# Kernel tuning notes

Hardware: AMD Instinct MI355X
Metric: run time of the kernel (lower is better)

The kernel has to match this reference:

```python
import jax, jax.numpy as jnp
import numpy as np

B, S, IN, OUT, SPLIT = 4, 2048, 4096, 4096, 1024


def setup_inputs() -> dict:
    key = jax.random.key(0)
    ks = jax.random.split(key, 14)
    def n(k, shape, scale=1.0):
        return jax.random.normal(k, shape, dtype=jnp.float32) * scale
    return {
        "x": n(ks[0], (B, S, IN)),
        "V": n(ks[1], (SPLIT, IN)),
        "U": n(ks[2], (OUT, SPLIT)),
        "v2": n(ks[3], (1, IN), 0.05),
        "v1": n(ks[4], (1, SPLIT), 0.05),
        "u2": n(ks[5], (1, SPLIT), 0.05),
        "u1": n(ks[6], (1, OUT), 0.05),
        "V_R": n(ks[7], (SPLIT, IN)),
        "U_R": n(ks[8], (OUT, SPLIT)),
        "v2_R": n(ks[9], (1, IN), 0.05),
        "v1_R": n(ks[10], (1, SPLIT), 0.05),
        "u2_R": n(ks[11], (1, SPLIT), 0.05),
        "u1_R": n(ks[12], (1, OUT), 0.05),
        "bias": n(ks[13], (OUT,), 0.02),
    }


def _quantize(w):
    # ITQ binarization: sign(w) with straight-through estimator semantics
    return w + jax.lax.stop_gradient(jnp.sign(w) - w)


def _compute_forward(x2d, V, U, v2, v1, u2, u1):
    # x2d: [T, in]; V: [split, in]; U: [out, split]
    Vq = _quantize(V)
    Uq = _quantize(U)
    v1u2 = v1 * u2  # [1, split]
    h = (x2d * v2) @ Vq.T          # [T, split]
    return (h * v1u2) @ Uq.T * u1  # [T, out]


def reference(x, V, U, v2, v1, u2, u1, V_R, U_R, v2_R, v1_R, u2_R, u1_R, bias):
    lead = x.shape[:-1]
    x2d = x.reshape(-1, x.shape[-1])
    y = _compute_forward(x2d, V, U, v2, v1, u2, u1)
    y = y + _compute_forward(x2d, V_R, U_R, v2_R, v1_R, u2_R, u1_R)
    y = y + bias
    return y.reshape(lead + (U.shape[0],))
```

## Files before the change

kernel.cpp:

```cpp
#include <hip/hip_runtime.h>


typedef __bf16 bf16x8 __attribute__((ext_vector_type(8)));
typedef float floatx4 __attribute__((ext_vector_type(4)));

__device__ __forceinline__ unsigned short f2bf_rne(float f) {
    union { float f; unsigned u; } v; v.f = f;
    unsigned r = v.u + 0x7FFFu + ((v.u >> 16) & 1u);
    return (unsigned short)(r >> 16);
}

__device__ __forceinline__ float sgnf(float w) {
    return (float)((w > 0.f) - (w < 0.f));
}

__device__ __forceinline__ void async_copy16(const void* g, void* l) {
    __builtin_amdgcn_global_load_lds(
        (const __attribute__((address_space(1))) void*)g,
        (__attribute__((address_space(3))) void*)l, 16, 0, 0);
}

#define FENCE() asm volatile("" ::: "memory")
#define BAR() do { FENCE(); __builtin_amdgcn_s_barrier(); FENCE(); } while (0)
#define VMW(N) asm volatile("s_waitcnt vmcnt(" #N ")" ::: "memory")
#define LGKM(N) asm volatile("s_waitcnt lgkmcnt(" #N ")" ::: "memory")


__global__ void prep_all_kernel(const float* __restrict__ x,
                                unsigned short* __restrict__ xb,
                                const float* __restrict__ V, const float* __restrict__ V_R,
                                const float* __restrict__ v2, const float* __restrict__ v2_R,
                                const float* __restrict__ U, const float* __restrict__ U_R,
                                const float* __restrict__ v1, const float* __restrict__ v1_R,
                                const float* __restrict__ u2, const float* __restrict__ u2_R,
                                const float* __restrict__ u1, const float* __restrict__ u1_R,
                                unsigned short* __restrict__ W1,
                                unsigned short* __restrict__ W2) {
    int bid = blockIdx.x;
    if (bid < 32768) {
        int i = bid * blockDim.x + threadIdx.x;
        float4 v = ((const float4*)x)[i];
        ushort4 o;
        o.x = f2bf_rne(v.x); o.y = f2bf_rne(v.y);
        o.z = f2bf_rne(v.z); o.w = f2bf_rne(v.w);
        ((ushort4*)xb)[i] = o;
    } else if (bid < 40960) {
        int i = (bid - 32768) * blockDim.x + threadIdx.x;
        int idx = i << 2;
        int scat = idx >> 12;
        int k = idx & 4095;
        const float* Vp; const float* sp;
        if (scat < 1024) { Vp = V + ((size_t)scat << 12); sp = v2; }
        else             { Vp = V_R + ((size_t)(scat - 1024) << 12); sp = v2_R; }
        float4 w = *(const float4*)(Vp + k);
        float4 s = *(const float4*)(sp + k);
        ushort4 o;
        o.x = f2bf_rne(sgnf(w.x) * s.x);
        o.y = f2bf_rne(sgnf(w.y) * s.y);
        o.z = f2bf_rne(sgnf(w.z) * s.z);
        o.w = f2bf_rne(sgnf(w.w) * s.w);
        ((ushort4*)W1)[i] = o;
    } else {
        int i = (bid - 40960) * blockDim.x + threadIdx.x;
        int idx = i << 2;
        int o = idx >> 11;
        int scat = idx & 2047;
        int branch = scat >> 10;
        int s = scat & 1023;
        const float* Up  = branch ? U_R  : U;
        const float* v1p = branch ? v1_R : v1;
        const float* u2p = branch ? u2_R : u2;
        float u1v = (branch ? u1_R : u1)[o];
        float4 w = *(const float4*)(Up + ((size_t)o << 10) + s);
        float4 a = *(const float4*)(v1p + s);
        float4 b = *(const float4*)(u2p + s);
        ushort4 out;
        out.x = f2bf_rne(sgnf(w.x) * a.x * b.x * u1v);
        out.y = f2bf_rne(sgnf(w.y) * a.y * b.y * u1v);
        out.z = f2bf_rne(sgnf(w.z) * a.z * b.z * u1v);
        out.w = f2bf_rne(sgnf(w.w) * a.w * b.w * u1v);
        ((ushort4*)W2)[i] = out;
    }
}


template <bool OUT_BF16, bool ADD_BIAS>
__global__ __launch_bounds__(512, 2)
void gemm256(const unsigned short* __restrict__ A,
             const unsigned short* __restrict__ B,
             void* __restrict__ Cv,
             const float* __restrict__ bias,
             int M, int N, int K, int ntn) {
    (void)M;
    __shared__ __align__(16) unsigned short As[2][2][128 * 64];
    __shared__ __align__(16) unsigned short Bs[2][2][128 * 64];

    const int tid = threadIdx.x;
    const int lane = tid & 63;
    const int wave = tid >> 6;
    const int warp_m = wave >> 2;
    const int warp_n = wave & 3;

    const int nwg = gridDim.x;
    const int hw = blockIdx.x;
    const int swz = (hw & 7) * (nwg >> 3) + (hw >> 3);
    const int tm = swz / ntn;
    const int tn = swz - tm * ntn;
    const int m0 = tm << 8;
    const int n0 = tn << 8;

    const int srow = tid >> 3;
    const int scg8 = (((tid & 7) ^ (srow & 7)) << 3);
    const int ldst = tid << 3;
    const size_t Ks = (size_t)K;

    auto stA = [&](int buf, int h, int kt) {
        const unsigned short* g = A + (size_t)(m0 + (h << 7) + srow) * Ks + (kt << 6) + scg8;
        async_copy16(g,             &As[buf][h][ldst]);
        async_copy16(g + (Ks << 6), &As[buf][h][4096 + ldst]);
    };
    auto stB = [&](int buf, int h, int kt) {
        const unsigned short* g = B + (size_t)(n0 + (h << 7) + srow) * Ks + (kt << 6) + scg8;
        async_copy16(g,             &Bs[buf][h][ldst]);
        async_copy16(g + (Ks << 6), &Bs[buf][h][4096 + ldst]);
    };

    const int fm = lane & 15;
    const int cgl = lane >> 4;
    const int key = fm & 7;
    const int ok0 = ((cgl ^ key) << 3);
    const int ok1 = (((4 | cgl) ^ key) << 3);

    auto lda = [&](bf16x8 (&dst)[4][2], int buf, int mh) {
        const unsigned short* base = &As[buf][warp_m][0];
#pragma unroll
        for (int mi = 0; mi < 4; ++mi) {
            const unsigned short* p = base + (((mh << 6) + (mi << 4) + fm) << 6);
            dst[mi][0] = *(const bf16x8*)(p + ok0);
            dst[mi][1] = *(const bf16x8*)(p + ok1);
        }
    };
    auto ldb = [&](bf16x8 (&dst)[2][2], int buf, int nh) {
        const unsigned short* base = &Bs[buf][warp_n >> 1][0];
#pragma unroll
        for (int ni = 0; ni < 2; ++ni) {
            const unsigned short* p = base + ((((warp_n & 1) << 6) + (nh << 5) + (ni << 4) + fm) << 6);
            dst[ni][0] = *(const bf16x8*)(p + ok0);
            dst[ni][1] = *(const bf16x8*)(p + ok1);
        }
    };

    floatx4 acc[8][4];
#pragma unroll
    for (int i = 0; i < 8; ++i)
#pragma unroll
        for (int j = 0; j < 4; ++j)
#pragma unroll
            for (int r = 0; r < 4; ++r) acc[i][j][r] = 0.f;

    bf16x8 a0[4][2], a1[4][2], b0[2][2], b1[2][2];

#define MMAQ(aS, bS, MH, NH) do { \
    __builtin_amdgcn_s_setprio(1); \
    _Pragma("unroll") \
    for (int mi_ = 0; mi_ < 4; ++mi_) { \
      _Pragma("unroll") \
      for (int ni_ = 0; ni_ < 2; ++ni_) { \
        acc[(MH)*4 + mi_][(NH)*2 + ni_] = __builtin_amdgcn_mfma_f32_16x16x32_bf16( \
            aS[mi_][0], bS[ni_][0], acc[(MH)*4 + mi_][(NH)*2 + ni_], 0, 0, 0); \
        acc[(MH)*4 + mi_][(NH)*2 + ni_] = __builtin_amdgcn_mfma_f32_16x16x32_bf16( \
            aS[mi_][1], bS[ni_][1], acc[(MH)*4 + mi_][(NH)*2 + ni_], 0, 0, 0); \
      } } \
    __builtin_amdgcn_s_setprio(0); \
  } while (0)

    stB(0, 0, 0); stB(0, 1, 0); stA(0, 0, 0); stA(0, 1, 0);
    stB(1, 0, 1); stB(1, 1, 1);
    VMW(4);
    BAR();

    const int NT = K >> 6;
    for (int i = 0; i < (NT >> 1) - 1; ++i) {
        const int t1k = 2 * i + 1, t2k = 2 * i + 2, t3k = 2 * i + 3;
        lda(a0, 0, 0); ldb(b0, 0, 0);
        stA(1, 0, t1k);
        LGKM(8);
        BAR(); LGKM(0);
        MMAQ(a0, b0, 0, 0);
        BAR();
        ldb(b1, 0, 1);
        stA(1, 1, t1k);
        BAR(); LGKM(0);
        MMAQ(a0, b1, 0, 1);
        BAR();
        lda(a1, 0, 1);
        stB(0, 0, t2k);
        BAR(); LGKM(0);
        MMAQ(a1, b1, 1, 1);
        BAR();
        stB(0, 1, t2k);
        VMW(4);
        BAR();
        MMAQ(a1, b0, 1, 0);
        BAR();
        lda(a0, 1, 0); ldb(b0, 1, 0);
        stA(0, 0, t2k);
        LGKM(8);
        BAR(); LGKM(0);
        MMAQ(a0, b0, 0, 0);
        BAR();
        ldb(b1, 1, 1);
        stA(0, 1, t2k);
        BAR(); LGKM(0);
        MMAQ(a0, b1, 0, 1);
        BAR();
        lda(a1, 1, 1);
        stB(1, 0, t3k);
        BAR(); LGKM(0);
        MMAQ(a1, b1, 1, 1);
        BAR();
        stB(1, 1, t3k);
        VMW(4);
        BAR();
        MMAQ(a1, b0, 1, 0);
        BAR();
    }
    {
        const int tLk = NT - 1;
        lda(a0, 0, 0); ldb(b0, 0, 0);
        stA(1, 0, tLk);
        LGKM(8);
        BAR(); LGKM(0);
        MMAQ(a0, b0, 0, 0);
        BAR();
        ldb(b1, 0, 1);
        stA(1, 1, tLk);
        BAR(); LGKM(0);
        MMAQ(a0, b1, 0, 1);
        BAR();
        lda(a1, 0, 1);
        BAR(); LGKM(0);
        MMAQ(a1, b1, 1, 1);
        BAR();
        VMW(0);
        BAR();
        MMAQ(a1, b0, 1, 0);
        BAR();
        lda(a0, 1, 0); ldb(b0, 1, 0);
        ldb(b1, 1, 1); lda(a1, 1, 1);
        MMAQ(a0, b0, 0, 0);
        MMAQ(a0, b1, 0, 1);
        MMAQ(a1, b1, 1, 1);
        MMAQ(a1, b0, 1, 0);
    }
#undef MMAQ

    const int rq = (lane >> 4) << 2;
    const int col = lane & 15;
#pragma unroll
    for (int mi = 0; mi < 8; ++mi) {
#pragma unroll
        for (int r = 0; r < 4; ++r) {
            const int gm = m0 + (warp_m << 7) + (mi << 4) + rq + r;
            const size_t base = (size_t)gm * (size_t)N;
#pragma unroll
            for (int ni = 0; ni < 4; ++ni) {
                const int gn = n0 + (warp_n << 6) + (ni << 4) + col;
                float v = acc[mi][ni][r];
                if (ADD_BIAS) v += bias[gn];
                if (OUT_BF16)
                    ((unsigned short*)Cv)[base + gn] = f2bf_rne(v);
                else
                    ((float*)Cv)[base + gn] = v;
            }
        }
    }
}


extern "C" void kernel_launch(void* const* d_in, const int* in_sizes, int n_in,
                              void* d_out, int out_size, void* d_ws, size_t ws_size,
                              hipStream_t stream) {
    const float* x    = (const float*)d_in[0];
    const float* V    = (const float*)d_in[1];
    const float* U    = (const float*)d_in[2];
    const float* v2   = (const float*)d_in[3];
    const float* v1   = (const float*)d_in[4];
    const float* u2   = (const float*)d_in[5];
    const float* u1   = (const float*)d_in[6];
    const float* V_R  = (const float*)d_in[7];
    const float* U_R  = (const float*)d_in[8];
    const float* v2_R = (const float*)d_in[9];
    const float* v1_R = (const float*)d_in[10];
    const float* u2_R = (const float*)d_in[11];
    const float* u1_R = (const float*)d_in[12];
    const float* bias = (const float*)d_in[13];
    float* out = (float*)d_out;

    char* ws = (char*)d_ws;
    unsigned short* Xb = (unsigned short*)ws;
    unsigned short* W1 = (unsigned short*)(ws + (size_t)67108864);
    unsigned short* W2 = (unsigned short*)(ws + (size_t)67108864 + 16777216);
    unsigned short* H  = (unsigned short*)(ws + (size_t)67108864 + 33554432);

    prep_all_kernel<<<49152, 256, 0, stream>>>(x, Xb, V, V_R, v2, v2_R,
                                               U, U_R, v1, v1_R, u2, u2_R, u1, u1_R,
                                               W1, W2);

    gemm256<true, false><<<dim3(256), 512, 0, stream>>>(Xb, W1, (void*)H, nullptr,
                                                        8192, 2048, 4096, 8);
    gemm256<false, true><<<dim3(512), 512, 0, stream>>>(H, W2, (void*)out, bias,
                                                        8192, 4096, 2048, 16);
}
```

Before: 531.9 us.

## Reorganize LDS half-tiles by quadrant and deepen async prefetch schedule

Changes the shared-memory layout so each A/B half-buffer holds the rows one MMA quadrant needs across all warps, rather than one warp's rows. This lets loads for the next k-tile be issued per quadrant earlier, with a deeper vmcnt window. It also drops one barrier per half-iteration by moving the wait after the last MMA quadrant. The interleaved load/compute ordering is more intricate, so any mistake in buffer reuse timing could race or stall.

```diff
diff --git a/kernel.cpp b/kernel.cpp
--- a/kernel.cpp
+++ b/kernel.cpp
@@ -114,15 +114,16 @@
     const int ldst = tid << 3;
     const size_t Ks = (size_t)K;
 
-    auto stA = [&](int buf, int h, int kt) {
-        const unsigned short* g = A + (size_t)(m0 + (h << 7) + srow) * Ks + (kt << 6) + scg8;
-        async_copy16(g,             &As[buf][h][ldst]);
-        async_copy16(g + (Ks << 6), &As[buf][h][4096 + ldst]);
+    auto stA = [&](int buf, int mh, int kt) {
+        const unsigned short* g = A + (size_t)(m0 + (mh << 6) + srow) * Ks + (kt << 6) + scg8;
+        async_copy16(g,             &As[buf][mh][ldst]);
+        async_copy16(g + (Ks << 7), &As[buf][mh][4096 + ldst]);
     };
-    auto stB = [&](int buf, int h, int kt) {
-        const unsigned short* g = B + (size_t)(n0 + (h << 7) + srow) * Ks + (kt << 6) + scg8;
-        async_copy16(g,             &Bs[buf][h][ldst]);
-        async_copy16(g + (Ks << 6), &Bs[buf][h][4096 + ldst]);
+    auto stB = [&](int buf, int nh, int kt) {
+        const unsigned short* g = B + (size_t)(n0 + ((srow >> 5) << 6) + (nh << 5) + (srow & 31)) * Ks
+                                    + (kt << 6) + scg8;
+        async_copy16(g,             &Bs[buf][nh][ldst]);
+        async_copy16(g + (Ks << 7), &Bs[buf][nh][4096 + ldst]);
     };
 
     const int fm = lane & 15;
@@ -132,19 +133,19 @@
     const int ok1 = (((4 | cgl) ^ key) << 3);
 
     auto lda = [&](bf16x8 (&dst)[4][2], int buf, int mh) {
-        const unsigned short* base = &As[buf][warp_m][0];
+        const unsigned short* base = &As[buf][mh][0];
 #pragma unroll
         for (int mi = 0; mi < 4; ++mi) {
-            const unsigned short* p = base + (((mh << 6) + (mi << 4) + fm) << 6);
+            const unsigned short* p = base + (((warp_m << 6) + (mi << 4) + fm) << 6);
             dst[mi][0] = *(const bf16x8*)(p + ok0);
             dst[mi][1] = *(const bf16x8*)(p + ok1);
         }
     };
     auto ldb = [&](bf16x8 (&dst)[2][2], int buf, int nh) {
-        const unsigned short* base = &Bs[buf][warp_n >> 1][0];
+        const unsigned short* base = &Bs[buf][nh][0];
 #pragma unroll
         for (int ni = 0; ni < 2; ++ni) {
-            const unsigned short* p = base + ((((warp_n & 1) << 6) + (nh << 5) + (ni << 4) + fm) << 6);
+            const unsigned short* p = base + (((warp_n << 5) + (ni << 4) + fm) << 6);
             dst[ni][0] = *(const bf16x8*)(p + ok0);
             dst[ni][1] = *(const bf16x8*)(p + ok1);
         }
@@ -174,67 +175,63 @@
     __builtin_amdgcn_s_setprio(0); \
   } while (0)
 
-    stB(0, 0, 0); stB(0, 1, 0); stA(0, 0, 0); stA(0, 1, 0);
-    stB(1, 0, 1); stB(1, 1, 1);
-    VMW(4);
+    stB(0, 0, 0); stA(0, 0, 0); stB(0, 1, 0); stA(0, 1, 0);
+    stB(1, 0, 1); stA(1, 0, 1); stB(1, 1, 1);
+    VMW(6);
     BAR();
 
     const int NT = K >> 6;
     for (int i = 0; i < (NT >> 1) - 1; ++i) {
-        const int t1k = 2 * i + 1, t2k = 2 * i + 2, t3k = 2 * i + 3;
+        const int ok = 2 * i + 1, fk = 2 * i + 2, gk = 2 * i + 3;
         lda(a0, 0, 0); ldb(b0, 0, 0);
-        stA(1, 0, t1k);
+        stA(1, 1, ok);
         LGKM(8);
         BAR(); LGKM(0);
         MMAQ(a0, b0, 0, 0);
         BAR();
         ldb(b1, 0, 1);
-        stA(1, 1, t1k);
+        stB(0, 0, fk);
         BAR(); LGKM(0);
         MMAQ(a0, b1, 0, 1);
         BAR();
         lda(a1, 0, 1);
-        stB(0, 0, t2k);
+        stA(0, 0, fk);
         BAR(); LGKM(0);
         MMAQ(a1, b1, 1, 1);
         BAR();
-        stB(0, 1, t2k);
-        VMW(4);
-        BAR();
+        stB(0, 1, fk);
         MMAQ(a1, b0, 1, 0);
+        VMW(6);
         BAR();
         lda(a0, 1, 0); ldb(b0, 1, 0);
-        stA(0, 0, t2k);
+        stA(0, 1, fk);
         LGKM(8);
         BAR(); LGKM(0);
         MMAQ(a0, b0, 0, 0);
         BAR();
         ldb(b1, 1, 1);
-        stA(0, 1, t2k);
+        stB(1, 0, gk);
         BAR(); LGKM(0);
         MMAQ(a0, b1, 0, 1);
         BAR();
         lda(a1, 1, 1);
-        stB(1, 0, t3k);
+        stA(1, 0, gk);
         BAR(); LGKM(0);
         MMAQ(a1, b1, 1, 1);
         BAR();
-        stB(1, 1, t3k);
-        VMW(4);
-        BAR();
+        stB(1, 1, gk);
         MMAQ(a1, b0, 1, 0);
+        VMW(6);
         BAR();
     }
     {
-        const int tLk = NT - 1;
         lda(a0, 0, 0); ldb(b0, 0, 0);
-        stA(1, 0, tLk);
+        stA(1, 1, NT - 1);
         LGKM(8);
         BAR(); LGKM(0);
         MMAQ(a0, b0, 0, 0);
         BAR();
         ldb(b1, 0, 1);
-        stA(1, 1, tLk);
         BAR(); LGKM(0);
         MMAQ(a0, b1, 0, 1);
         BAR();
@@ -242,9 +239,8 @@
         BAR(); LGKM(0);
         MMAQ(a1, b1, 1, 1);
         BAR();
+        MMAQ(a1, b0, 1, 0);
         VMW(0);
-        BAR();
-        MMAQ(a1, b0, 1, 0);
         BAR();
         lda(a0, 1, 0); ldb(b0, 1, 0);
         ldb(b1, 1, 1); lda(a1, 1, 1);
```

Result: no change. 532.8 us (+0.2%).
